# Optimization experiments

Hardware: AMD Instinct MI355X
Metric: run time of the kernel (lower is better)

## Reference

```python
import jax, jax.numpy as jnp
import numpy as np

B, T, L, IN, D, H = 2, 16, 256, 768, 1024, 16
HD = D // H
NREG = 4
P = NREG + 2          # frozen prefix: registers + noise + action
DEPTH = 8
TINT = 4              # temporal_attention_interval
CTX = 30              # temporal_context_length
BASE = 1000.0         # rope_base
EPS = 1e-6            # qk_norm_eps / rmsnorm eps
HID = 4096            # 4.0 * latent_dim
S = L + P             # tokens per frame


def _rms(x, w=None, eps=EPS):
    y = x * jax.lax.rsqrt(jnp.mean(x * x, axis=-1, keepdims=True) + eps)
    return y * w if w is not None else y


def _rope_cache(n, hd, base):
    inv = base ** (-jnp.arange(0, hd, 2, dtype=jnp.float32) / hd)
    ang = jnp.arange(n, dtype=jnp.float32)[:, None] * inv[None, :]  # [n, hd/2]
    return jnp.cos(ang), jnp.sin(ang)


def _apply_rope(x, cos, sin):
    x1, x2 = x[..., ::2], x[..., 1::2]
    return jnp.stack([x1 * cos - x2 * sin, x1 * sin + x2 * cos], axis=-1).reshape(x.shape)


def _attn(x, Wqkv, Wo, cos, sin, mask):
    # x: [..., S, D]; mask: bool, True = attend, broadcastable to [..., H, S, S]
    qkv = x @ Wqkv
    q, k, v = jnp.split(qkv, 3, axis=-1)
    heads = lambda t: t.reshape(t.shape[:-1] + (H, HD)).swapaxes(-2, -3)  # [..., H, S, HD]
    q, k, v = heads(q), heads(k), heads(v)
    q = _apply_rope(_rms(q), cos, sin)   # qk-norm then RoPE
    k = _apply_rope(_rms(k), cos, sin)
    s = jnp.einsum('...qd,...kd->...qk', q, k) / jnp.sqrt(jnp.float32(HD))
    s = jnp.where(mask, s, jnp.float32(-1e9))
    p = jax.nn.softmax(s, axis=-1) * mask.any(axis=-1, keepdims=True)  # zero rows with no allowed keys
    o = jnp.einsum('...qk,...kd->...qd', p, v)
    return o.swapaxes(-2, -3).reshape(x.shape) @ Wo


def _spatial_mask():
    m = np.zeros((S, S), bool)
    r, n, a, ls = NREG, NREG, NREG + 1, NREG + 2
    m[ls:, ls:] = True; m[ls:, n] = True; m[ls:, a] = True; m[ls:, :r] = True
    m[n, n] = True; m[a, a] = True
    m[:r, ls:] = True; m[:r, n] = True; m[:r, a] = True; m[:r, :r] = True
    return jnp.asarray(m)


def _temporal_mask(indep):
    m = jnp.tril(jnp.ones((T, T), bool), -1)  # strictly-past causal
    if CTX is not None and CTX < T:
        m = m & jnp.triu(m, -CTX)             # sliding context window
    m = jnp.broadcast_to(m, (B, T, T))
    m = jnp.where(indep[:, None, None], False, m)
    return m[:, None, None]  # [B,1,1,T,T] -> broadcasts over token pos and heads


def setup_inputs() -> dict:
    key = jax.random.key(0)
    ks = iter(jax.random.split(key, 40))
    g = lambda shape, s=0.02: jax.random.normal(next(ks), shape, jnp.float32) * s
    inp = {
        'noisy_latents': jax.random.normal(next(ks), (B, T, L, IN), jnp.float32),
        'noise_levels': jax.random.uniform(next(ks), (B, T), jnp.float32),
        'actions': jax.random.normal(next(ks), (B, T, 6), jnp.float32),
        'independent_frames_mask': jnp.zeros((B,), bool),
        'actions_mask': jnp.ones((B, T), bool),
        'W_in': g((IN, D)),
        'noise_w1': g((1, D)), 'noise_b1': jnp.zeros((D,), jnp.float32),
        'noise_w2': g((D, D)), 'noise_b2': jnp.zeros((D,), jnp.float32),
        'base_action_embed': g((D,)),
        'action_w': g((6, D)), 'action_b': jnp.zeros((D,), jnp.float32),
        'registers': g((NREG, D)),
        'ln1_w': jnp.ones((DEPTH, D), jnp.float32),
        'Wqkv_s': g((DEPTH, D, 3 * D)), 'Wo_s': g((DEPTH, D, D)),
        'lnt_w': jnp.ones((DEPTH, D), jnp.float32),
        'Wqkv_t': g((DEPTH, D, 3 * D)), 'Wo_t': g((DEPTH, D, D)),
        'ln2_w': jnp.ones((DEPTH, D), jnp.float32),
        'W1': g((DEPTH, D, HID)), 'W2': g((DEPTH, D, HID)), 'W3': g((DEPTH, HID, D)),
        'final_w': jnp.ones((D,), jnp.float32),
        'W_out': g((D, IN)), 'b_out': jnp.zeros((IN,), jnp.float32),
    }
    return inp


def reference(noisy_latents, noise_levels, actions, independent_frames_mask, actions_mask,
              W_in, noise_w1, noise_b1, noise_w2, noise_b2, base_action_embed,
              action_w, action_b, registers, ln1_w, Wqkv_s, Wo_s, lnt_w, Wqkv_t, Wo_t,
              ln2_w, W1, W2, W3, final_w, W_out, b_out):
    noisy_tokens = noisy_latents @ W_in                                   # [B,T,L,D]
    base = jnp.broadcast_to(base_action_embed, (B, T, 1, D))
    act = base + (actions @ action_w + action_b)[:, :, None, :]
    act = jnp.where(actions_mask[:, :, None, None], act, base)            # [B,T,1,D]
    nz = jax.nn.silu(noise_levels[..., None] @ noise_w1 + noise_b1) @ noise_w2 + noise_b2
    nz = nz[:, :, None, :]                                                # [B,T,1,D]
    reg = jnp.broadcast_to(registers, (B, T, NREG, D))
    x = jnp.concatenate([reg, nz, act, noisy_tokens], axis=2)             # [B,T,S,D]

    sp_mask = _spatial_mask()
    tm_mask = _temporal_mask(independent_frames_mask)
    sp_cos, sp_sin = _rope_cache(S, HD, BASE)
    tm_cos, tm_sin = _rope_cache(T, HD, BASE)
    keep_tok = (jnp.arange(S) >= P)[None, :, None, None]                  # zero temporal update on frozen prefix

    for i in range(DEPTH):
        h = _rms(x, ln1_w[i])
        x = x + _attn(h, Wqkv_s[i], Wo_s[i], sp_cos, sp_sin, sp_mask)
        if i % TINT == 0:
            ht = _rms(x, lnt_w[i]).transpose(0, 2, 1, 3)                  # [B,S,T,D]
            ot = _attn(ht, Wqkv_t[i], Wo_t[i], tm_cos, tm_sin, tm_mask)
            x = x + (ot * keep_tok).transpose(0, 2, 1, 3)
        h2 = _rms(x, ln2_w[i])
        x = x + (jax.nn.silu(h2 @ W1[i]) * (h2 @ W2[i])) @ W3[i]

    latents = _rms(x[..., P:, :], final_w)
    pred_clean_latents = latents @ W_out + b_out                          # [B,T,L,IN]
    return pred_clean_latents
```

## Files before the change

### kernel.cpp

```cpp
#include <hip/hip_runtime.h>
#include <cstdint>
#include <cstddef>

#define DEV __device__ __forceinline__

typedef __attribute__((ext_vector_type(8))) __bf16 bf16x8;
typedef __attribute__((ext_vector_type(4))) float f32x4;

#define NTOK   8384
#define NTOKP  8448
#define NLAT   8192

DEV float b2f(unsigned short u) {
  unsigned int x = ((unsigned int)u) << 16;
  return __builtin_bit_cast(float, x);
}
DEV unsigned short f2b(float f) {
  unsigned int x = __builtin_bit_cast(unsigned int, f);
  x += 0x7fffu + ((x >> 16) & 1u);
  return (unsigned short)(x >> 16);
}
DEV float wred_sum(float v) {
#pragma unroll
  for (int o = 32; o; o >>= 1) v += __shfl_xor(v, o);
  return v;
}
DEV bool mask_or(const void* p, int i) {
  return ((const unsigned char*)p)[i] != 0 || ((const int*)p)[i] != 0;
}
DEV bool mask_and(const void* p, int i) {
  return ((const unsigned char*)p)[i] != 0 && ((const int*)p)[i] != 0;
}


__global__ void conv_f2b(const float* __restrict__ in, unsigned short* __restrict__ out, int n4) {
  int i = blockIdx.x * 256 + threadIdx.x;
  if (i < n4) {
    float4 v = ((const float4*)in)[i];
    ushort4 o;
    o.x = f2b(v.x); o.y = f2b(v.y); o.z = f2b(v.z); o.w = f2b(v.w);
    ((ushort4*)out)[i] = o;
  }
}

__global__ void build_rope(float2* __restrict__ out, int npos) {
  int idx = blockIdx.x * 256 + threadIdx.x;
  if (idx >= npos * 32) return;
  int pos = idx >> 5, i = idx & 31;
  float inv = powf(1000.0f, -(float)(2 * i) * (1.0f / 64.0f));
  float ang = (float)pos * inv;
  float sv, cv;
  sincosf(ang, &sv, &cv);
  out[idx] = make_float2(cv, sv);
}

__global__ __launch_bounds__(256) void transpose_w(const float* __restrict__ in,
                                                   unsigned short* __restrict__ out,
                                                   int K, int N, int ostride, int mode) {
  __shared__ float tile[32][33];
  int kb = blockIdx.x * 32, nb = blockIdx.y * 32;
  int tx = threadIdx.x & 31, ty = threadIdx.x >> 5;
#pragma unroll
  for (int i = 0; i < 32; i += 8)
    tile[ty + i][tx] = in[(size_t)(kb + ty + i) * N + (nb + tx)];
  __syncthreads();
#pragma unroll
  for (int i = 0; i < 32; i += 8) {
    int n = nb + ty + i;
    int row = n;
    if (mode == 1) row = ((n >> 4) << 5) | (n & 15);
    else if (mode == 2) row = (((n >> 4) << 5) + 16) | (n & 15);
    out[(size_t)row * ostride + (kb + tx)] = f2b(tile[tx][ty + i]);
  }
}

__global__ __launch_bounds__(256) void noise_h1(const float* __restrict__ nlvl,
                                                const float* __restrict__ w1,
                                                const float* __restrict__ b1,
                                                const float* __restrict__ b2,
                                                float* __restrict__ h1,
                                                float* __restrict__ nz) {
  int i = blockIdx.x * 256 + threadIdx.x;
  int bt = i >> 10, d = i & 1023;
  float v = nlvl[bt] * w1[d] + b1[d];
  h1[i] = v / (1.0f + expf(-v));
  nz[i] = b2[d];
}

__global__ __launch_bounds__(256) void noise_mm(const float* __restrict__ h1,
                                                const float* __restrict__ w2,
                                                float* __restrict__ nz) {
  __shared__ float hs[32][128];
  int kc = blockIdx.x >> 4, dpg = blockIdx.x & 15;
  int tid = threadIdx.x;
  int k0 = kc * 128;
  for (int idx = tid; idx < 32 * 128; idx += 256) {
    int bt = idx >> 7, k = idx & 127;
    hs[bt][k] = h1[bt * 1024 + k0 + k];
  }
  __syncthreads();
  int dp = dpg * 64 + (tid & 63);
  int bt0 = (tid >> 6) * 8;
  float acc[8] = {};
  for (int k = 0; k < 128; ++k) {
    float w = w2[(size_t)(k0 + k) * 1024 + dp];
#pragma unroll
    for (int j = 0; j < 8; ++j) acc[j] += hs[bt0 + j][k] * w;
  }
#pragma unroll
  for (int j = 0; j < 8; ++j) atomicAdd(&nz[(bt0 + j) * 1024 + dp], acc[j]);
}

__global__ void embed_special(float* __restrict__ x, const float* __restrict__ regs,
                              const float* __restrict__ nz, const float* __restrict__ base_emb,
                              const float* __restrict__ actions, const float* __restrict__ action_w,
                              const float* __restrict__ action_b,
                              const void* __restrict__ amask) {
  int bt = blockIdx.x, d = threadIdx.x;
  float* xr = x + (size_t)bt * 262 * 1024;
#pragma unroll
  for (int r = 0; r < 4; ++r) xr[r * 1024 + d] = regs[r * 1024 + d];
  xr[4 * 1024 + d] = nz[(size_t)bt * 1024 + d];
  float a = base_emb[d];
  if (mask_or(amask, bt)) {
    float s = action_b[d];
#pragma unroll
    for (int i = 0; i < 6; ++i) s += actions[bt * 6 + i] * action_w[i * 1024 + d];
    a += s;
  }
  xr[5 * 1024 + d] = a;
}

template <bool REMAP>
__global__ __launch_bounds__(256) void rms_k(const float* __restrict__ x,
                                             const float* __restrict__ w,
                                             unsigned short* __restrict__ out) {
  int m = blockIdx.x, tid = threadIdx.x;
  size_t src = REMAP ? ((size_t)(m >> 8) * 262 + 6 + (m & 255)) : (size_t)m;
  float4 v = ((const float4*)(x + src * 1024))[tid];
  float ss = v.x * v.x + v.y * v.y + v.z * v.z + v.w * v.w;
  ss = wred_sum(ss);
  __shared__ float sred[4];
  if ((tid & 63) == 0) sred[tid >> 6] = ss;
  __syncthreads();
  float tot = sred[0] + sred[1] + sred[2] + sred[3];
  float sc = rsqrtf(tot * (1.0f / 1024.0f) + 1e-6f);
  float4 wv = ((const float4*)w)[tid];
  ushort4 o;
  o.x = f2b(v.x * sc * wv.x); o.y = f2b(v.y * sc * wv.y);
  o.z = f2b(v.z * sc * wv.z); o.w = f2b(v.w * sc * wv.w);
  ((ushort4*)(out + (size_t)m * 1024))[tid] = o;
}

#define KSTR 72
#define VSTR 296
__global__ __launch_bounds__(256) void attn_spatial(const unsigned short* __restrict__ qkv,
                                                    unsigned short* __restrict__ o,
                                                    const float2* __restrict__ rope) {
  __shared__ unsigned short Ks[272 * KSTR];
  __shared__ unsigned short Vt[64 * VSTR];
  __shared__ unsigned short Ps[4][16 * VSTR];
  const int h = blockIdx.x & 15;
  const int bt = blockIdx.x >> 4;
  const int tid = threadIdx.x, wave = tid >> 6, lane = tid & 63;
  const size_t tb = (size_t)bt * 262;

  {
    const int d = lane;
#pragma unroll 1
    for (int pss = 0; pss < 17; ++pss) {
      const int t0 = (pss * 4 + wave) * 4;
      ushort4 vp;
      unsigned short* vpp = (unsigned short*)&vp;
#pragma unroll
      for (int j = 0; j < 4; ++j) {
        const int t = t0 + j;
        float kv = 0.f, vv = 0.f;
        if (t < 262) {
          const size_t rb = (tb + t) * 3072 + h * 64 + d;
          kv = b2f(qkv[rb + 1024]);
          vv = b2f(qkv[rb + 2048]);
        }
        float ss = wred_sum(kv * kv);
        kv *= rsqrtf(ss * (1.0f / 64.0f) + 1e-6f);
        float partner = __shfl_xor(kv, 1);
        const int tc = t < 262 ? t : 261;
        float2 cs = rope[tc * 32 + (d >> 1)];
        kv = ((d & 1) == 0) ? (kv * cs.x - partner * cs.y)
                            : (partner * cs.y + kv * cs.x);
        Ks[t * KSTR + d] = f2b(kv);
        vpp[j] = f2b(vv);
      }
      *(ushort4*)(&Vt[d * VSTR + t0]) = vp;
    }
    for (int idx = tid; idx < 64 * 24; idx += 256) {
      Vt[(idx / 24) * VSTR + 272 + (idx % 24)] = 0;
    }
    for (int idx = tid; idx < 4 * 16 * 34; idx += 256) {
      int w = idx / (16 * 34), r = (idx / 34) & 15, c = idx % 34;
      Ps[w][r * VSTR + 262 + c] = 0;
    }
  }
  __syncthreads();

  unsigned short* Pw = &Ps[wave][0];
  const int kcol = lane & 15;
  const int g8 = (lane >> 4) << 3;
  const int g4 = g8 >> 1;
  const int rq = (lane >> 4) << 2;

#pragma unroll 1
  for (int qc = wave; qc < 17; qc += 4) {
    const int q0 = qc * 16;
    const int qrow = q0 + kcol;
    const int grow = qrow < 262 ? qrow : 261;
    const unsigned short* qp = qkv + (tb + grow) * 3072 + h * 64 + g8;
    float qv[16];
    {
      ushort4 a = *(const ushort4*)qp, b = *(const ushort4*)(qp + 4);
      ushort4 c = *(const ushort4*)(qp + 32), e = *(const ushort4*)(qp + 36);
      qv[0] = b2f(a.x); qv[1] = b2f(a.y); qv[2] = b2f(a.z); qv[3] = b2f(a.w);
      qv[4] = b2f(b.x); qv[5] = b2f(b.y); qv[6] = b2f(b.z); qv[7] = b2f(b.w);
      qv[8] = b2f(c.x); qv[9] = b2f(c.y); qv[10] = b2f(c.z); qv[11] = b2f(c.w);
      qv[12] = b2f(e.x); qv[13] = b2f(e.y); qv[14] = b2f(e.z); qv[15] = b2f(e.w);
    }
    float ss = 0.f;
#pragma unroll
    for (int i = 0; i < 16; ++i) ss += qv[i] * qv[i];
    ss += __shfl_xor(ss, 16);
    ss += __shfl_xor(ss, 32);
    const float qsc = rsqrtf(ss * (1.0f / 64.0f) + 1e-6f);
    bf16x8 aq0, aq1;
    unsigned short* u0 = (unsigned short*)&aq0;
    unsigned short* u1 = (unsigned short*)&aq1;
#pragma unroll
    for (int i = 0; i < 4; ++i) {
      float2 cs0 = rope[grow * 32 + g4 + i];
      float a = qv[2 * i] * qsc, b = qv[2 * i + 1] * qsc;
      u0[2 * i] = f2b(a * cs0.x - b * cs0.y);
      u0[2 * i + 1] = f2b(a * cs0.y + b * cs0.x);
      float2 cs1 = rope[grow * 32 + 16 + g4 + i];
      float a1 = qv[8 + 2 * i] * qsc, b1 = qv[9 + 2 * i] * qsc;
      u1[2 * i] = f2b(a1 * cs1.x - b1 * cs1.y);
      u1[2 * i + 1] = f2b(a1 * cs1.y + b1 * cs1.x);
    }
    f32x4 sc[17];
#pragma unroll
    for (int kc = 0; kc < 17; ++kc) {
      const unsigned short* kb = &Ks[(kc * 16 + kcol) * KSTR + g8];
      f32x4 z = {};
      z = __builtin_amdgcn_mfma_f32_16x16x32_bf16(aq0, *(const bf16x8*)kb, z, 0, 0, 0);
      sc[kc] = __builtin_amdgcn_mfma_f32_16x16x32_bf16(aq1, *(const bf16x8*)(kb + 32), z, 0, 0, 0);
    }
#pragma unroll
    for (int kc = 0; kc < 17; ++kc) {
      const int k = kc * 16 + kcol;
#pragma unroll
      for (int j = 0; j < 4; ++j) {
        const int sq = q0 + rq + j;
        const bool valid = (k < 262) && ((sq != 4 && sq != 5) || (k == sq));
        sc[kc][j] = valid ? sc[kc][j] * 0.125f : -1e30f;
      }
    }
    float sm[4];
#pragma unroll
    for (int j = 0; j < 4; ++j) {
      float m = -1e30f;
#pragma unroll
      for (int kc = 0; kc < 17; ++kc) m = fmaxf(m, sc[kc][j]);
#pragma unroll
      for (int off = 1; off < 16; off <<= 1) m = fmaxf(m, __shfl_xor(m, off));
      float s = 0.f;
#pragma unroll
      for (int kc = 0; kc < 17; ++kc) {
        float e = expf(sc[kc][j] - m);
        sc[kc][j] = e;
        s += e;
      }
#pragma unroll
      for (int off = 1; off < 16; off <<= 1) s += __shfl_xor(s, off);
      sm[j] = 1.0f / s;
    }
#pragma unroll
    for (int kc = 0; kc < 17; ++kc) {
      const int k = kc * 16 + kcol;
#pragma unroll
      for (int j = 0; j < 4; ++j)
        Pw[(rq + j) * VSTR + k] = f2b(sc[kc][j] * sm[j]);
    }
    f32x4 oacc[4] = {};
#pragma unroll
    for (int tc = 0; tc < 9; ++tc) {
      const bf16x8 ap = *(const bf16x8*)(&Pw[kcol * VSTR + tc * 32 + g8]);
#pragma unroll
      for (int nt = 0; nt < 4; ++nt) {
        const bf16x8 bv = *(const bf16x8*)(&Vt[(nt * 16 + kcol) * VSTR + tc * 32 + g8]);
        oacc[nt] = __builtin_amdgcn_mfma_f32_16x16x32_bf16(ap, bv, oacc[nt], 0, 0, 0);
      }
    }
#pragma unroll
    for (int nt = 0; nt < 4; ++nt) {
#pragma unroll
      for (int j = 0; j < 4; ++j) {
        const int sq = q0 + rq + j;
        if (sq < 262)
          o[(tb + sq) * 1024 + h * 64 + nt * 16 + kcol] = f2b(oacc[nt][j]);
      }
    }
  }
}

__global__ __launch_bounds__(256) void attn_temporal(const unsigned short* __restrict__ qkv,
                                                     unsigned short* __restrict__ o,
                                                     const float2* __restrict__ rope,
                                                     const void* __restrict__ indep) {
  int gw = blockIdx.x * 4 + (threadIdx.x >> 6);
  int lane = threadIdx.x & 63;
  if (gw >= NTOK) return;
  int h = gw & 15;
  int s = (gw >> 4) % 262;
  int b = (gw >> 4) / 262;
  bool dead = (s < 6) || mask_and(indep, b);
  float q[16], kk[16], vv[16], out[16];
#pragma unroll
  for (int t = 0; t < 16; ++t) {
    out[t] = 0.f;
    if (!dead) {
      size_t off = ((size_t)((b * 16 + t) * 262 + s)) * 3072 + h * 64 + lane;
      q[t] = b2f(qkv[off]);
      kk[t] = b2f(qkv[off + 1024]);
      vv[t] = b2f(qkv[off + 2048]);
    }
  }
  if (!dead) {
#pragma unroll
    for (int t = 0; t < 16; ++t) {
      float sq_ = wred_sum(q[t] * q[t]);
      float qv = q[t] * rsqrtf(sq_ * (1.0f / 64.0f) + 1e-6f);
      float sk_ = wred_sum(kk[t] * kk[t]);
      float kv = kk[t] * rsqrtf(sk_ * (1.0f / 64.0f) + 1e-6f);
      float2 cs = rope[t * 32 + (lane >> 1)];
      float qp = __shfl_xor(qv, 1);
      float kp = __shfl_xor(kv, 1);
      q[t] = ((lane & 1) == 0) ? (qv * cs.x - qp * cs.y) : (qp * cs.y + qv * cs.x);
      kk[t] = ((lane & 1) == 0) ? (kv * cs.x - kp * cs.y) : (kp * cs.y + kv * cs.x);
    }
#pragma unroll
    for (int t = 1; t < 16; ++t) {
      float m = -1e30f, l = 0.f, acc = 0.f;
#pragma unroll
      for (int j = 0; j < t; ++j) {
        float pr = q[t] * kk[j];
#pragma unroll
        for (int o2 = 32; o2; o2 >>= 1) pr += __shfl_xor(pr, o2);
        pr *= 0.125f;
        float mn = fmaxf(m, pr);
        float cor = expf(m - mn);
        float e = expf(pr - mn);
        l = l * cor + e;
        acc = acc * cor + e * vv[j];
        m = mn;
      }
      out[t] = acc / l;
    }
  }
#pragma unroll
  for (int t = 0; t < 16; ++t) {
    size_t off = ((size_t)((b * 16 + t) * 262 + s)) * 1024 + h * 64 + lane;
    o[off] = f2b(out[t]);
  }
}

DEV void stage_tiles(const unsigned short* __restrict__ A, const unsigned short* __restrict__ Bw,
                     size_t arow0, size_t brow0, int lda, int k0,
                     unsigned short* As, unsigned short* Bs, int wave, int lane) {
  const int srow = lane >> 2;
  const int scol = (lane & 3) * 8;
#pragma unroll
  for (int c = 0; c < 2; ++c) {
    const int chunk = wave * 2 + c;
    unsigned short* ga = const_cast<unsigned short*>(A + (arow0 + chunk * 16 + srow) * lda + k0 + scol);
    unsigned short* gb = const_cast<unsigned short*>(Bw + (brow0 + chunk * 16 + srow) * lda + k0 + scol);
    __builtin_amdgcn_global_load_lds((__attribute__((address_space(1))) void*)ga,
                                     (__attribute__((address_space(3))) void*)(As + chunk * 512),
                                     16, 0, 0);
    __builtin_amdgcn_global_load_lds((__attribute__((address_space(1))) void*)gb,
                                     (__attribute__((address_space(3))) void*)(Bs + chunk * 512),
                                     16, 0, 0);
  }
}

template <int EPI>
__global__ __launch_bounds__(256) void gemm_k(const unsigned short* __restrict__ A,
                                              const unsigned short* __restrict__ Bw,
                                              void* __restrict__ C,
                                              const float* __restrict__ aux,
                                              int Mvalid, int K, int lda, int ldc) {
  __shared__ unsigned short As[2][128 * 32];
  __shared__ unsigned short Bs[2][128 * 32];
  const int tid = threadIdx.x;
  const int wave = tid >> 6, lane = tid & 63;
  const int wm = wave >> 1, wn = wave & 1;
  const size_t arow0 = (size_t)blockIdx.x * 128;
  const size_t brow0 = (size_t)blockIdx.y * 128;

  f32x4 acc[4][4] = {};
  const int KT = K >> 5;

  stage_tiles(A, Bw, arow0, brow0, lda, 0, As[0], Bs[0], wave, lane);
  __syncthreads();
  int buf = 0;
  for (int kt = 0; kt < KT; ++kt) {
    if (kt + 1 < KT)
      stage_tiles(A, Bw, arow0, brow0, lda, (kt + 1) << 5, As[buf ^ 1], Bs[buf ^ 1], wave, lane);
    const int kk = (lane >> 4) * 8;
    const int rsel = lane & 15;
    bf16x8 af[4], bfr[4];
#pragma unroll
    for (int mt = 0; mt < 4; ++mt)
      af[mt] = *reinterpret_cast<const bf16x8*>(&As[buf][(wm * 64 + mt * 16 + rsel) * 32 + kk]);
#pragma unroll
    for (int nt = 0; nt < 4; ++nt)
      bfr[nt] = *reinterpret_cast<const bf16x8*>(&Bs[buf][(wn * 64 + nt * 16 + rsel) * 32 + kk]);
#pragma unroll
    for (int mt = 0; mt < 4; ++mt) {
#pragma unroll
      for (int nt = 0; nt < 4; ++nt)
        acc[mt][nt] = __builtin_amdgcn_mfma_f32_16x16x32_bf16(af[mt], bfr[nt], acc[mt][nt], 0, 0, 0);
    }
    __syncthreads();
    buf ^= 1;
  }

  const int rsel = lane & 15;
  const int row_base = blockIdx.x * 128 + wm * 64;
  const int col_base = blockIdx.y * 128 + wn * 64;

  if (EPI == 2) {
    const int cg0 = blockIdx.y * 64 + wn * 32;
#pragma unroll
    for (int mt = 0; mt < 4; ++mt) {
#pragma unroll
      for (int pr = 0; pr < 2; ++pr) {
        const int col = cg0 + pr * 16 + rsel;
        const int r0 = row_base + mt * 16 + ((lane >> 4) << 2);
#pragma unroll
        for (int j = 0; j < 4; ++j) {
          const int row = r0 + j;
          if (row < Mvalid) {
            float u1 = acc[mt][pr * 2][j];
            float u2 = acc[mt][pr * 2 + 1][j];
            float sv = u1 / (1.0f + expf(-u1));
            ((unsigned short*)C)[(size_t)row * ldc + col] = f2b(sv * u2);
          }
        }
      }
    }
    return;
  }

#pragma unroll
  for (int mt = 0; mt < 4; ++mt) {
#pragma unroll
    for (int nt = 0; nt < 4; ++nt) {
      const int col = col_base + nt * 16 + rsel;
      const int r0 = row_base + mt * 16 + ((lane >> 4) << 2);
#pragma unroll
      for (int j = 0; j < 4; ++j) {
        const int row = r0 + j;
        float v = acc[mt][nt][j];
        if (row < Mvalid) {
          if (EPI == 0) {
            ((unsigned short*)C)[(size_t)row * ldc + col] = f2b(v);
          } else if (EPI == 1) {
            float* p = (float*)C + (size_t)row * ldc + col;
            *p += v;
          } else if (EPI == 3) {
            ((float*)C)[(size_t)row * ldc + col] = v + aux[col];
          } else if (EPI == 5) {
            int xr = (row >> 8) * 262 + 6 + (row & 255);
            ((float*)C)[(size_t)xr * ldc + col] = v;
          }
        }
      }
    }
  }
}

extern "C" void kernel_launch(void* const* d_in, const int* in_sizes, int n_in,
                              void* d_out, int out_size, void* d_ws, size_t ws_size,
                              hipStream_t stream) {
  const float* noisy = (const float*)d_in[0];
  const float* nlvl = (const float*)d_in[1];
  const float* actions = (const float*)d_in[2];
  const void* indep = d_in[3];
  const void* amask = d_in[4];
  const float* W_in = (const float*)d_in[5];
  const float* noise_w1 = (const float*)d_in[6];
  const float* noise_b1 = (const float*)d_in[7];
  const float* noise_w2 = (const float*)d_in[8];
  const float* noise_b2 = (const float*)d_in[9];
  const float* base_emb = (const float*)d_in[10];
  const float* action_w = (const float*)d_in[11];
  const float* action_b = (const float*)d_in[12];
  const float* registers = (const float*)d_in[13];
  const float* ln1_w = (const float*)d_in[14];
  const float* Wqkv_s = (const float*)d_in[15];
  const float* Wo_s = (const float*)d_in[16];
  const float* lnt_w = (const float*)d_in[17];
  const float* Wqkv_t = (const float*)d_in[18];
  const float* Wo_t = (const float*)d_in[19];
  const float* ln2_w = (const float*)d_in[20];
  const float* W1 = (const float*)d_in[21];
  const float* W2 = (const float*)d_in[22];
  const float* W3 = (const float*)d_in[23];
  const float* final_w = (const float*)d_in[24];
  const float* W_out = (const float*)d_in[25];
  const float* b_out = (const float*)d_in[26];

  char* p = (char*)d_ws;
  auto alloc = [&](size_t bytes) {
    char* r = p;
    p += (bytes + 255) & ~(size_t)255;
    return r;
  };
  float* X = (float*)alloc((size_t)NTOKP * 1024 * 4);
  unsigned short* HB = (unsigned short*)alloc((size_t)NTOKP * 1024 * 2);
  unsigned short* AO = (unsigned short*)alloc((size_t)NTOKP * 1024 * 2);
  char* SCR = alloc((size_t)NTOKP * 4096 * 2);
  unsigned short* QKV = (unsigned short*)SCR;
  unsigned short* G = (unsigned short*)SCR;
  unsigned short* NLB = (unsigned short*)SCR;
  float* NZ = (float*)alloc(32 * 1024 * 4);
  float* H1 = (float*)alloc(32 * 1024 * 4);
  float2* RSP = (float2*)alloc(262 * 32 * 8);
  float2* RTM = (float2*)alloc(16 * 32 * 8);
  unsigned short* WINT = (unsigned short*)alloc((size_t)1024 * 768 * 2);
  unsigned short* WQKVS = (unsigned short*)alloc((size_t)8 * 3072 * 1024 * 2);
  unsigned short* WOS = (unsigned short*)alloc((size_t)8 * 1024 * 1024 * 2);
  unsigned short* WQKVT = (unsigned short*)alloc((size_t)8 * 3072 * 1024 * 2);
  unsigned short* WOT = (unsigned short*)alloc((size_t)8 * 1024 * 1024 * 2);
  unsigned short* W12T = (unsigned short*)alloc((size_t)8 * 8192 * 1024 * 2);
  unsigned short* W3T = (unsigned short*)alloc((size_t)8 * 1024 * 4096 * 2);
  unsigned short* WOUTT = (unsigned short*)alloc((size_t)768 * 1024 * 2);

  auto tr = [&](const float* in, unsigned short* out, int K, int N, int ostride, int mode) {
    dim3 g(K / 32, N / 32);
    transpose_w<<<g, 256, 0, stream>>>(in, out, K, N, ostride, mode);
  };
  tr(W_in, WINT, 768, 1024, 768, 0);
  for (int i = 0; i < 8; ++i) {
    tr(Wqkv_s + (size_t)i * 1024 * 3072, WQKVS + (size_t)i * 3072 * 1024, 1024, 3072, 1024, 0);
    tr(Wo_s + (size_t)i * 1024 * 1024, WOS + (size_t)i * 1024 * 1024, 1024, 1024, 1024, 0);
    tr(Wqkv_t + (size_t)i * 1024 * 3072, WQKVT + (size_t)i * 3072 * 1024, 1024, 3072, 1024, 0);
    tr(Wo_t + (size_t)i * 1024 * 1024, WOT + (size_t)i * 1024 * 1024, 1024, 1024, 1024, 0);
    tr(W1 + (size_t)i * 1024 * 4096, W12T + (size_t)i * 8192 * 1024, 1024, 4096, 1024, 1);
    tr(W2 + (size_t)i * 1024 * 4096, W12T + (size_t)i * 8192 * 1024, 1024, 4096, 1024, 2);
    tr(W3 + (size_t)i * 4096 * 1024, W3T + (size_t)i * 1024 * 4096, 4096, 1024, 4096, 0);
  }
  tr(W_out, WOUTT, 1024, 768, 1024, 0);

  build_rope<<<33, 256, 0, stream>>>(RSP, 262);
  build_rope<<<2, 256, 0, stream>>>(RTM, 16);
  conv_f2b<<<6144, 256, 0, stream>>>(noisy, NLB, (NLAT * 768) / 4);
  noise_h1<<<128, 256, 0, stream>>>(nlvl, noise_w1, noise_b1, noise_b2, H1, NZ);
  noise_mm<<<128, 256, 0, stream>>>(H1, noise_w2, NZ);
  embed_special<<<32, 1024, 0, stream>>>(X, registers, NZ, base_emb, actions, action_w, action_b, amask);
  {
    dim3 g(64, 8);
    gemm_k<5><<<g, 256, 0, stream>>>(NLB, WINT, X, nullptr, NLAT, 768, 768, 1024);
  }

  for (int i = 0; i < 8; ++i) {
    rms_k<false><<<NTOK, 256, 0, stream>>>(X, ln1_w + i * 1024, HB);
    {
      dim3 g(66, 24);
      gemm_k<0><<<g, 256, 0, stream>>>(HB, WQKVS + (size_t)i * 3072 * 1024, QKV, nullptr, NTOK, 1024, 1024, 3072);
    }
    attn_spatial<<<512, 256, 0, stream>>>(QKV, AO, RSP);
    {
      dim3 g(66, 8);
      gemm_k<1><<<g, 256, 0, stream>>>(AO, WOS + (size_t)i * 1024 * 1024, X, nullptr, NTOK, 1024, 1024, 1024);
    }
    if ((i & 3) == 0) {
      rms_k<false><<<NTOK, 256, 0, stream>>>(X, lnt_w + i * 1024, HB);
      {
        dim3 g(66, 24);
        gemm_k<0><<<g, 256, 0, stream>>>(HB, WQKVT + (size_t)i * 3072 * 1024, QKV, nullptr, NTOK, 1024, 1024, 3072);
      }
      attn_temporal<<<2096, 256, 0, stream>>>(QKV, AO, RTM, indep);
      {
        dim3 g(66, 8);
        gemm_k<1><<<g, 256, 0, stream>>>(AO, WOT + (size_t)i * 1024 * 1024, X, nullptr, NTOK, 1024, 1024, 1024);
      }
    }
    rms_k<false><<<NTOK, 256, 0, stream>>>(X, ln2_w + i * 1024, HB);
    {
      dim3 g(66, 64);
      gemm_k<2><<<g, 256, 0, stream>>>(HB, W12T + (size_t)i * 8192 * 1024, G, nullptr, NTOK, 1024, 1024, 4096);
    }
    {
      dim3 g(66, 8);
      gemm_k<1><<<g, 256, 0, stream>>>(G, W3T + (size_t)i * 1024 * 4096, X, nullptr, NTOK, 4096, 4096, 1024);
    }
  }

  rms_k<true><<<NLAT, 256, 0, stream>>>(X, final_w, HB);
  {
    dim3 g(64, 6);
    gemm_k<3><<<g, 256, 0, stream>>>(HB, WOUTT, d_out, b_out, NLAT, 1024, 1024, 768);
  }
}
```

Before: 5.928 ms.

## Fuse RMSNorm into GEMM epilogues via per-row sum-of-squares accumulation

Drops the standalone rms_k kernels between layers. The RMSNorm weights are folded into the transposed weight matrices, and residual-update GEMM epilogues now write both the fp32 residual and an unnormalized bf16 copy. They also atomically accumulate per-row sums of squares into slot buffers, and the consumer GEMMs apply rsqrt scaling in their epilogue. This removes a full read of X and a write of HB per norm. In exchange it adds atomics and extra bf16 stores in the epilogues, and the bf16 operand is now unnormalized, which may change rounding.

```diff
diff --git a/kernel.cpp b/kernel.cpp
--- a/kernel.cpp
+++ b/kernel.cpp
@@ -10,6 +10,7 @@
 #define NTOK   8384
 #define NTOKP  8448
 #define NLAT   8192
+#define NSQS   18
 
 DEV float b2f(unsigned short u) {
   unsigned int x = ((unsigned int)u) << 16;
@@ -32,6 +33,11 @@
   return ((const unsigned char*)p)[i] != 0 && ((const int*)p)[i] != 0;
 }
 
+
+__global__ void zerof(float* __restrict__ p, int n) {
+  int i = blockIdx.x * 256 + threadIdx.x;
+  if (i < n) p[i] = 0.f;
+}
 
 __global__ void conv_f2b(const float* __restrict__ in, unsigned short* __restrict__ out, int n4) {
   int i = blockIdx.x * 256 + threadIdx.x;
@@ -56,13 +62,17 @@
 
 __global__ __launch_bounds__(256) void transpose_w(const float* __restrict__ in,
                                                    unsigned short* __restrict__ out,
-                                                   int K, int N, int ostride, int mode) {
+                                                   int K, int N, int ostride, int mode,
+                                                   const float* __restrict__ lnw) {
   __shared__ float tile[32][33];
   int kb = blockIdx.x * 32, nb = blockIdx.y * 32;
   int tx = threadIdx.x & 31, ty = threadIdx.x >> 5;
 #pragma unroll
-  for (int i = 0; i < 32; i += 8)
-    tile[ty + i][tx] = in[(size_t)(kb + ty + i) * N + (nb + tx)];
+  for (int i = 0; i < 32; i += 8) {
+    float v = in[(size_t)(kb + ty + i) * N + (nb + tx)];
+    if (lnw) v *= lnw[kb + ty + i];
+    tile[ty + i][tx] = v;
+  }
   __syncthreads();
 #pragma unroll
   for (int i = 0; i < 32; i += 8) {
@@ -111,16 +121,25 @@
   for (int j = 0; j < 8; ++j) atomicAdd(&nz[(bt0 + j) * 1024 + dp], acc[j]);
 }
 
-__global__ void embed_special(float* __restrict__ x, const float* __restrict__ regs,
+__global__ void embed_special(float* __restrict__ x, unsigned short* __restrict__ hb,
+                              float* __restrict__ sq0,
+                              const float* __restrict__ regs,
                               const float* __restrict__ nz, const float* __restrict__ base_emb,
                               const float* __restrict__ actions, const float* __restrict__ action_w,
                               const float* __restrict__ action_b,
                               const void* __restrict__ amask) {
   int bt = blockIdx.x, d = threadIdx.x;
-  float* xr = x + (size_t)bt * 262 * 1024;
-#pragma unroll
-  for (int r = 0; r < 4; ++r) xr[r * 1024 + d] = regs[r * 1024 + d];
-  xr[4 * 1024 + d] = nz[(size_t)bt * 1024 + d];
+  const int lane = d & 63;
+  auto put = [&](int r, float val) {
+    size_t row = (size_t)bt * 262 + r;
+    x[row * 1024 + d] = val;
+    hb[row * 1024 + d] = f2b(val);
+    float ss = wred_sum(val * val);
+    if (lane == 0) atomicAdd(sq0 + row, ss);
+  };
+#pragma unroll
+  for (int r = 0; r < 4; ++r) put(r, regs[r * 1024 + d]);
+  put(4, nz[(size_t)bt * 1024 + d]);
   float a = base_emb[d];
   if (mask_or(amask, bt)) {
     float s = action_b[d];
@@ -128,15 +147,14 @@
     for (int i = 0; i < 6; ++i) s += actions[bt * 6 + i] * action_w[i * 1024 + d];
     a += s;
   }
-  xr[5 * 1024 + d] = a;
-}
-
-template <bool REMAP>
-__global__ __launch_bounds__(256) void rms_k(const float* __restrict__ x,
-                                             const float* __restrict__ w,
-                                             unsigned short* __restrict__ out) {
+  put(5, a);
+}
+
+__global__ __launch_bounds__(256) void rms_final(const float* __restrict__ x,
+                                                 const float* __restrict__ w,
+                                                 unsigned short* __restrict__ out) {
   int m = blockIdx.x, tid = threadIdx.x;
-  size_t src = REMAP ? ((size_t)(m >> 8) * 262 + 6 + (m & 255)) : (size_t)m;
+  size_t src = (size_t)(m >> 8) * 262 + 6 + (m & 255);
   float4 v = ((const float4*)(x + src * 1024))[tid];
   float ss = v.x * v.x + v.y * v.y + v.z * v.z + v.w * v.w;
   ss = wred_sum(ss);
@@ -394,7 +412,8 @@
 __global__ __launch_bounds__(256) void gemm_k(const unsigned short* __restrict__ A,
                                               const unsigned short* __restrict__ Bw,
                                               void* __restrict__ C,
-                                              const float* __restrict__ aux,
+                                              void* __restrict__ C2,
+                                              float* __restrict__ aux,
                                               int Mvalid, int K, int lda, int ldc) {
   __shared__ unsigned short As[2][128 * 32];
   __shared__ unsigned short Bs[2][128 * 32];
@@ -436,24 +455,53 @@
   const int row_base = blockIdx.x * 128 + wm * 64;
   const int col_base = blockIdx.y * 128 + wn * 64;
 
-  if (EPI == 2) {
+  if (EPI == 9) {
     const int cg0 = blockIdx.y * 64 + wn * 32;
 #pragma unroll
     for (int mt = 0; mt < 4; ++mt) {
-#pragma unroll
-      for (int pr = 0; pr < 2; ++pr) {
-        const int col = cg0 + pr * 16 + rsel;
-        const int r0 = row_base + mt * 16 + ((lane >> 4) << 2);
-#pragma unroll
-        for (int j = 0; j < 4; ++j) {
-          const int row = r0 + j;
+      const int r0 = row_base + mt * 16 + ((lane >> 4) << 2);
+#pragma unroll
+      for (int j = 0; j < 4; ++j) {
+        const int row = r0 + j;
+        if (row >= Mvalid) continue;
+        const float s = rsqrtf(aux[row] * (1.0f / 1024.0f) + 1e-6f);
+#pragma unroll
+        for (int pr = 0; pr < 2; ++pr) {
+          const int col = cg0 + pr * 16 + rsel;
+          float u1 = acc[mt][pr * 2][j] * s;
+          float u2 = acc[mt][pr * 2 + 1][j] * s;
+          float sv = u1 / (1.0f + expf(-u1));
+          ((unsigned short*)C)[(size_t)row * ldc + col] = f2b(sv * u2);
+        }
+      }
+    }
+    return;
+  }
+
+  if (EPI == 7 || EPI == 10) {
+#pragma unroll
+    for (int mt = 0; mt < 4; ++mt) {
+      const int r0 = row_base + mt * 16 + ((lane >> 4) << 2);
+#pragma unroll
+      for (int j = 0; j < 4; ++j) {
+        const int row = r0 + j;
+        const int xr = (EPI == 10) ? ((row >> 8) * 262 + 6 + (row & 255)) : row;
+        float t = 0.f;
+#pragma unroll
+        for (int nt = 0; nt < 4; ++nt) {
+          const int col = col_base + nt * 16 + rsel;
+          float xn = 0.f;
           if (row < Mvalid) {
-            float u1 = acc[mt][pr * 2][j];
-            float u2 = acc[mt][pr * 2 + 1][j];
-            float sv = u1 / (1.0f + expf(-u1));
-            ((unsigned short*)C)[(size_t)row * ldc + col] = f2b(sv * u2);
+            float* p = (float*)C + (size_t)xr * ldc + col;
+            xn = (EPI == 7) ? (*p + acc[mt][nt][j]) : acc[mt][nt][j];
+            *p = xn;
+            ((unsigned short*)C2)[(size_t)xr * ldc + col] = f2b(xn);
           }
+          t += xn * xn;
         }
+        t += __shfl_xor(t, 1); t += __shfl_xor(t, 2);
+        t += __shfl_xor(t, 4); t += __shfl_xor(t, 8);
+        if (rsel == 0 && row < Mvalid) atomicAdd(aux + xr, t);
       }
     }
     return;
@@ -470,16 +518,14 @@
         const int row = r0 + j;
         float v = acc[mt][nt][j];
         if (row < Mvalid) {
-          if (EPI == 0) {
-            ((unsigned short*)C)[(size_t)row * ldc + col] = f2b(v);
-          } else if (EPI == 1) {
+          if (EPI == 1) {
             float* p = (float*)C + (size_t)row * ldc + col;
             *p += v;
           } else if (EPI == 3) {
             ((float*)C)[(size_t)row * ldc + col] = v + aux[col];
-          } else if (EPI == 5) {
-            int xr = (row >> 8) * 262 + 6 + (row & 255);
-            ((float*)C)[(size_t)xr * ldc + col] = v;
+          } else if (EPI == 8) {
+            const float s = rsqrtf(aux[row] * (1.0f / 1024.0f) + 1e-6f);
+            ((unsigned short*)C)[(size_t)row * ldc + col] = f2b(v * s);
           }
         }
       }
@@ -531,6 +577,7 @@
   unsigned short* QKV = (unsigned short*)SCR;
   unsigned short* G = (unsigned short*)SCR;
   unsigned short* NLB = (unsigned short*)SCR;
+  float* SQS = (float*)alloc((size_t)NSQS * NTOKP * 4);
   float* NZ = (float*)alloc(32 * 1024 * 4);
   float* H1 = (float*)alloc(32 * 1024 * 4);
   float2* RSP = (float2*)alloc(262 * 32 * 8);
@@ -538,76 +585,87 @@
   unsigned short* WINT = (unsigned short*)alloc((size_t)1024 * 768 * 2);
   unsigned short* WQKVS = (unsigned short*)alloc((size_t)8 * 3072 * 1024 * 2);
   unsigned short* WOS = (unsigned short*)alloc((size_t)8 * 1024 * 1024 * 2);
-  unsigned short* WQKVT = (unsigned short*)alloc((size_t)8 * 3072 * 1024 * 2);
-  unsigned short* WOT = (unsigned short*)alloc((size_t)8 * 1024 * 1024 * 2);
+  unsigned short* WQKVT = (unsigned short*)alloc((size_t)2 * 3072 * 1024 * 2);
+  unsigned short* WOT = (unsigned short*)alloc((size_t)2 * 1024 * 1024 * 2);
   unsigned short* W12T = (unsigned short*)alloc((size_t)8 * 8192 * 1024 * 2);
   unsigned short* W3T = (unsigned short*)alloc((size_t)8 * 1024 * 4096 * 2);
   unsigned short* WOUTT = (unsigned short*)alloc((size_t)768 * 1024 * 2);
 
-  auto tr = [&](const float* in, unsigned short* out, int K, int N, int ostride, int mode) {
+  auto SQ = [&](int slot) { return SQS + (size_t)slot * NTOKP; };
+
+  auto tr = [&](const float* in, unsigned short* out, int K, int N, int ostride, int mode,
+                const float* lnw) {
     dim3 g(K / 32, N / 32);
-    transpose_w<<<g, 256, 0, stream>>>(in, out, K, N, ostride, mode);
+    transpose_w<<<g, 256, 0, stream>>>(in, out, K, N, ostride, mode, lnw);
   };
-  tr(W_in, WINT, 768, 1024, 768, 0);
+  tr(W_in, WINT, 768, 1024, 768, 0, nullptr);
   for (int i = 0; i < 8; ++i) {
-    tr(Wqkv_s + (size_t)i * 1024 * 3072, WQKVS + (size_t)i * 3072 * 1024, 1024, 3072, 1024, 0);
-    tr(Wo_s + (size_t)i * 1024 * 1024, WOS + (size_t)i * 1024 * 1024, 1024, 1024, 1024, 0);
-    tr(Wqkv_t + (size_t)i * 1024 * 3072, WQKVT + (size_t)i * 3072 * 1024, 1024, 3072, 1024, 0);
-    tr(Wo_t + (size_t)i * 1024 * 1024, WOT + (size_t)i * 1024 * 1024, 1024, 1024, 1024, 0);
-    tr(W1 + (size_t)i * 1024 * 4096, W12T + (size_t)i * 8192 * 1024, 1024, 4096, 1024, 1);
-    tr(W2 + (size_t)i * 1024 * 4096, W12T + (size_t)i * 8192 * 1024, 1024, 4096, 1024, 2);
-    tr(W3 + (size_t)i * 4096 * 1024, W3T + (size_t)i * 1024 * 4096, 4096, 1024, 4096, 0);
-  }
-  tr(W_out, WOUTT, 1024, 768, 1024, 0);
-
+    tr(Wqkv_s + (size_t)i * 1024 * 3072, WQKVS + (size_t)i * 3072 * 1024, 1024, 3072, 1024, 0, ln1_w + i * 1024);
+    tr(Wo_s + (size_t)i * 1024 * 1024, WOS + (size_t)i * 1024 * 1024, 1024, 1024, 1024, 0, nullptr);
+    tr(W1 + (size_t)i * 1024 * 4096, W12T + (size_t)i * 8192 * 1024, 1024, 4096, 1024, 1, ln2_w + i * 1024);
+    tr(W2 + (size_t)i * 1024 * 4096, W12T + (size_t)i * 8192 * 1024, 1024, 4096, 1024, 2, ln2_w + i * 1024);
+    tr(W3 + (size_t)i * 4096 * 1024, W3T + (size_t)i * 1024 * 4096, 4096, 1024, 4096, 0, nullptr);
+  }
+  for (int s = 0; s < 2; ++s) {
+    int i = s * 4;
+    tr(Wqkv_t + (size_t)i * 1024 * 3072, WQKVT + (size_t)s * 3072 * 1024, 1024, 3072, 1024, 0, lnt_w + i * 1024);
+    tr(Wo_t + (size_t)i * 1024 * 1024, WOT + (size_t)s * 1024 * 1024, 1024, 1024, 1024, 0, nullptr);
+  }
+  tr(W_out, WOUTT, 1024, 768, 1024, 0, nullptr);
+
+  zerof<<<(NSQS * NTOKP + 255) / 256, 256, 0, stream>>>(SQS, NSQS * NTOKP);
   build_rope<<<33, 256, 0, stream>>>(RSP, 262);
   build_rope<<<2, 256, 0, stream>>>(RTM, 16);
   conv_f2b<<<6144, 256, 0, stream>>>(noisy, NLB, (NLAT * 768) / 4);
   noise_h1<<<128, 256, 0, stream>>>(nlvl, noise_w1, noise_b1, noise_b2, H1, NZ);
   noise_mm<<<128, 256, 0, stream>>>(H1, noise_w2, NZ);
-  embed_special<<<32, 1024, 0, stream>>>(X, registers, NZ, base_emb, actions, action_w, action_b, amask);
+  embed_special<<<32, 1024, 0, stream>>>(X, HB, SQ(0), registers, NZ, base_emb, actions, action_w, action_b, amask);
   {
     dim3 g(64, 8);
-    gemm_k<5><<<g, 256, 0, stream>>>(NLB, WINT, X, nullptr, NLAT, 768, 768, 1024);
+    gemm_k<10><<<g, 256, 0, stream>>>(NLB, WINT, X, HB, SQ(0), NLAT, 768, 768, 1024);
   }
 
   for (int i = 0; i < 8; ++i) {
-    rms_k<false><<<NTOK, 256, 0, stream>>>(X, ln1_w + i * 1024, HB);
+    const int sl_ln1 = i;
+    const int sl_after_wos = (i == 0) ? 8 : (i == 4) ? 9 : (10 + i);
+    const int sl_ln2 = 10 + i;
     {
       dim3 g(66, 24);
-      gemm_k<0><<<g, 256, 0, stream>>>(HB, WQKVS + (size_t)i * 3072 * 1024, QKV, nullptr, NTOK, 1024, 1024, 3072);
+      gemm_k<8><<<g, 256, 0, stream>>>(HB, WQKVS + (size_t)i * 3072 * 1024, QKV, nullptr, SQ(sl_ln1), NTOK, 1024, 1024, 3072);
     }
     attn_spatial<<<512, 256, 0, stream>>>(QKV, AO, RSP);
     {
       dim3 g(66, 8);
-      gemm_k<1><<<g, 256, 0, stream>>>(AO, WOS + (size_t)i * 1024 * 1024, X, nullptr, NTOK, 1024, 1024, 1024);
+      gemm_k<7><<<g, 256, 0, stream>>>(AO, WOS + (size_t)i * 1024 * 1024, X, HB, SQ(sl_after_wos), NTOK, 1024, 1024, 1024);
     }
     if ((i & 3) == 0) {
-      rms_k<false><<<NTOK, 256, 0, stream>>>(X, lnt_w + i * 1024, HB);
+      const int s = i >> 2;
       {
         dim3 g(66, 24);
-        gemm_k<0><<<g, 256, 0, stream>>>(HB, WQKVT + (size_t)i * 3072 * 1024, QKV, nullptr, NTOK, 1024, 1024, 3072);
+        gemm_k<8><<<g, 256, 0, stream>>>(HB, WQKVT + (size_t)s * 3072 * 1024, QKV, nullptr, SQ(8 + s), NTOK, 1024, 1024, 3072);
       }
       attn_temporal<<<2096, 256, 0, stream>>>(QKV, AO, RTM, indep);
       {
         dim3 g(66, 8);
-        gemm_k<1><<<g, 256, 0, stream>>>(AO, WOT + (size_t)i * 1024 * 1024, X, nullptr, NTOK, 1024, 1024, 1024);
-      }
-    }
-    rms_k<false><<<NTOK, 256, 0, stream>>>(X, ln2_w + i * 1024, HB);
+        gemm_k<7><<<g, 256, 0, stream>>>(AO, WOT + (size_t)s * 1024 * 1024, X, HB, SQ(sl_ln2), NTOK, 1024, 1024, 1024);
+      }
+    }
     {
       dim3 g(66, 64);
-      gemm_k<2><<<g, 256, 0, stream>>>(HB, W12T + (size_t)i * 8192 * 1024, G, nullptr, NTOK, 1024, 1024, 4096);
+      gemm_k<9><<<g, 256, 0, stream>>>(HB, W12T + (size_t)i * 8192 * 1024, G, nullptr, SQ(sl_ln2), NTOK, 1024, 1024, 4096);
     }
     {
       dim3 g(66, 8);
-      gemm_k<1><<<g, 256, 0, stream>>>(G, W3T + (size_t)i * 1024 * 4096, X, nullptr, NTOK, 4096, 4096, 1024);
-    }
-  }
-
-  rms_k<true><<<NLAT, 256, 0, stream>>>(X, final_w, HB);
+      if (i < 7)
+        gemm_k<7><<<g, 256, 0, stream>>>(G, W3T + (size_t)i * 1024 * 4096, X, HB, SQ(i + 1), NTOK, 4096, 4096, 1024);
+      else
+        gemm_k<1><<<g, 256, 0, stream>>>(G, W3T + (size_t)i * 1024 * 4096, X, nullptr, nullptr, NTOK, 4096, 4096, 1024);
+    }
+  }
+
+  rms_final<<<NLAT, 256, 0, stream>>>(X, final_w, HB);
   {
     dim3 g(64, 6);
-    gemm_k<3><<<g, 256, 0, stream>>>(HB, WOUTT, d_out, b_out, NLAT, 1024, 1024, 768);
-  }
-}
+    gemm_k<3><<<g, 256, 0, stream>>>(HB, WOUTT, d_out, nullptr, const_cast<float*>(b_out), NLAT, 1024, 1024, 768);
+  }
+}
```

After: 6.220 ms. 1.05x slower.
